# Performance work log

Hardware: AMD Instinct MI355X
Metric: run time of the kernel (lower is better)

Reference implementation:

```python
import jax, jax.numpy as jnp
import numpy as np

N = 10000        # nodes
F_IN = 128       # node features (data.num_node_features)
OUT = 16         # out_channels
H = 32           # attention heads
C1 = 4 * OUT     # hidden per-head dim (4*out_channels)
E = 80000        # directed edges
EPS = 1e-5       # BatchNorm eps
NEG = 0.2        # GATConv LeakyReLU negative_slope


def _gat(x, src, dst, W, a_s, a_d, b, n, C):
    # PyG GATConv, shared lin, concat=False (mean over heads)
    h = (x @ W).reshape(n, H, C)                    # [n,H,C]
    e_src = jnp.sum(h * a_s, -1)                    # [n,H] (alpha from x_j)
    e_dst = jnp.sum(h * a_d, -1)                    # [n,H] (alpha from x_i)
    e = jax.nn.leaky_relu(e_src[src] + e_dst[dst], NEG)     # [E',H]
    m = jax.ops.segment_max(e, dst, num_segments=n)         # segment softmax
    p = jnp.exp(e - m[dst])
    z = jax.ops.segment_sum(p, dst, num_segments=n)
    alpha = p / z[dst]
    out = jax.ops.segment_sum(alpha[:, :, None] * h[src], dst, num_segments=n)
    return out.mean(1) + b                          # mean over heads + bias


def _bn(x, g, b, m, v):  # eval-mode BatchNorm1d (running stats)
    return (x - m) * g / jnp.sqrt(v + EPS) + b


def setup_inputs():
    k = jax.random.split(jax.random.key(0), 40)
    rn = lambda i, s, sc=0.1: jax.random.normal(k[i], s, jnp.float32) * sc
    d = {"x": jax.random.normal(k[0], (N, F_IN), jnp.float32),
         "edge_index": jax.random.randint(k[1], (2, E), 0, N, jnp.int32)}
    # 4 GATConv layers
    d.update(W1=rn(2, (F_IN, H * C1)), as1=rn(3, (H, C1)), ad1=rn(4, (H, C1)), b1=rn(5, (C1,)))
    d.update(W2=rn(6, (C1, H * OUT)), as2=rn(7, (H, OUT)), ad2=rn(8, (H, OUT)), b2=rn(9, (OUT,)))
    d.update(W3=rn(10, (F_IN, H * C1)), as3=rn(11, (H, C1)), ad3=rn(12, (H, C1)), b3=rn(13, (C1,)))
    d.update(W4=rn(14, (C1, H * OUT)), as4=rn(15, (H, OUT)), ad4=rn(16, (H, OUT)), b4=rn(17, (OUT,)))
    # ResidualNetwork(1 block): 1x1 Conv1d over L=1 == matmul
    d.update(rwa=rn(18, (F_IN, OUT)), rba=rn(19, (OUT,)),
             bn1g=jnp.ones(OUT), bn1b=jnp.zeros(OUT), bn1m=rn(20, (OUT,)), bn1v=jnp.abs(rn(21, (OUT,))) + 1.0,
             rwb=rn(22, (OUT, OUT)), rbb=rn(23, (OUT,)),
             bn2g=jnp.ones(OUT), bn2b=jnp.zeros(OUT), bn2m=rn(24, (OUT,)), bn2v=jnp.abs(rn(25, (OUT,))) + 1.0,
             wsc=rn(26, (F_IN, OUT)), bsc=rn(27, (OUT,)),
             bnsg=jnp.ones(OUT), bnsb=jnp.zeros(OUT), bnsm=rn(28, (OUT,)), bnsv=jnp.abs(rn(29, (OUT,))) + 1.0,
             wfc=rn(30, (OUT, OUT)), bfc=rn(31, (OUT,)))
    return d


def reference(x, edge_index, W1, as1, ad1, b1, W2, as2, ad2, b2,
              W3, as3, ad3, b3, W4, as4, ad4, b4,
              rwa, rba, bn1g, bn1b, bn1m, bn1v, rwb, rbb, bn2g, bn2b, bn2m, bn2v,
              wsc, bsc, bnsg, bnsb, bnsm, bnsv, wfc, bfc):
    n = x.shape[0]
    loops = jnp.arange(n, dtype=edge_index.dtype)  # add_self_loops=True
    s2t_src = jnp.concatenate([edge_index[0], loops])  # flow source_to_target
    s2t_dst = jnp.concatenate([edge_index[1], loops])
    t2s_src = jnp.concatenate([edge_index[1], loops])  # flow target_to_source
    t2s_dst = jnp.concatenate([edge_index[0], loops])
    # dropout in original is unassigned (no-op); eval mode assumed
    x_s = jax.nn.elu(_gat(x, s2t_src, s2t_dst, W1, as1, ad1, b1, n, C1))
    x_in = jax.nn.elu(_gat(x_s, s2t_src, s2t_dst, W2, as2, ad2, b2, n, OUT))
    x_t = jax.nn.elu(_gat(x, t2s_src, t2s_dst, W3, as3, ad3, b3, n, C1))
    x_out = jax.nn.elu(_gat(x_t, t2s_src, t2s_dst, W4, as4, ad4, b4, n, OUT))
    # ResidualNetwork: block + identity avg-pool (L=1) + fc
    h = jax.nn.relu(_bn(x @ rwa + rba, bn1g, bn1b, bn1m, bn1v))
    h = _bn(h @ rwb + rbb, bn2g, bn2b, bn2m, bn2v)
    sc = _bn(x @ wsc + bsc, bnsg, bnsb, bnsm, bnsv)
    x_self = jax.nn.relu(h + sc) @ wfc + bfc
    return (x_in, x_out, x_self)
```

## Files before the change

### kernel.cpp

```cpp
#include <hip/hip_runtime.h>
#include <stdint.h>

__device__ __forceinline__ float bf2f(unsigned short u) {
  union { unsigned int i; float f; } v; v.i = ((unsigned int)u) << 16; return v.f;
}
__device__ __forceinline__ unsigned short f2bf(float f) {
  union { float f; unsigned int i; } v; v.f = f;
  unsigned int i = v.i;
  unsigned int r = (i + 0x7fffu + ((i >> 16) & 1u)) >> 16;
  return (unsigned short)r;
}

typedef __bf16 bf16x8 __attribute__((ext_vector_type(8)));
typedef float f32x4 __attribute__((ext_vector_type(4)));
typedef float f32x2 __attribute__((ext_vector_type(2)));
union ABfrag { int4 i4; bf16x8 v; };

#if __has_builtin(__builtin_amdgcn_cvt_pk_fp8_f32) && __has_builtin(__builtin_amdgcn_cvt_pk_f32_fp8)
#define HW_FP8 1
#else
#define HW_FP8 0
#endif

__device__ __forceinline__ unsigned char f2fp8_sw(float f) {
  union { float f; unsigned int u; } v; v.f = f;
  unsigned int s = (v.u >> 24) & 0x80;
  float a = fabsf(f);
  if (a >= 448.f) return (unsigned char)(s | 0x7E);
  v.f = a;
  int ex = (int)(v.u >> 23);
  unsigned int man = v.u & 0x7FFFFFu;
  if (ex >= 121) {
    unsigned int val = ((unsigned int)(ex - 120) << 3) | (man >> 20);
    unsigned int rem = man & 0xFFFFFu;
    if (rem > 0x80000u || (rem == 0x80000u && (val & 1))) val++;
    if (val > 0x7E) val = 0x7E;
    return (unsigned char)(s | val);
  }
  int q = (int)(a * 512.f + 0.5f);
  if (q > 8) q = 8;
  return (unsigned char)(s | (unsigned int)q);
}
__device__ __forceinline__ float fp8dec_sw(unsigned char c) {
  unsigned int e = (c >> 3) & 15u, m = c & 7u;
  float v;
  if (e) { union { unsigned int u; float f; } x; x.u = ((e + 120) << 23) | (m << 20); v = x.f; }
  else v = (float)m * 0.001953125f;
  return (c & 0x80) ? -v : v;
}
__device__ __forceinline__ unsigned int pack4_fp8(float a0, float a1, float a2, float a3) {
#if HW_FP8
  int dw = __builtin_amdgcn_cvt_pk_fp8_f32(a0, a1, 0, false);
  dw = __builtin_amdgcn_cvt_pk_fp8_f32(a2, a3, dw, true);
  return (unsigned int)dw;
#else
  return (unsigned)f2fp8_sw(a0) | ((unsigned)f2fp8_sw(a1) << 8) |
         ((unsigned)f2fp8_sw(a2) << 16) | ((unsigned)f2fp8_sw(a3) << 24);
#endif
}
__device__ __forceinline__ unsigned int bytesel4(uint4 v, int rr) {
#if __has_builtin(__builtin_amdgcn_perm)
  unsigned s = (unsigned)rr | ((unsigned)(rr + 4) << 8);
  unsigned p01 = __builtin_amdgcn_perm(v.y, v.x, s);
  unsigned p23 = __builtin_amdgcn_perm(v.w, v.z, s);
  return __builtin_amdgcn_perm(p23, p01, 0x05040100u);
#else
  int sh = rr * 8;
  return ((v.x >> sh) & 0xFFu) | (((v.y >> sh) & 0xFFu) << 8) |
         (((v.z >> sh) & 0xFFu) << 16) | (((v.w >> sh) & 0xFFu) << 24);
#endif
}
__device__ __forceinline__ void dec16p(int4 g, f32x2 o[8]) {
#if HW_FP8
  o[0] = __builtin_amdgcn_cvt_pk_f32_fp8(g.x, false);
  o[1] = __builtin_amdgcn_cvt_pk_f32_fp8(g.x, true);
  o[2] = __builtin_amdgcn_cvt_pk_f32_fp8(g.y, false);
  o[3] = __builtin_amdgcn_cvt_pk_f32_fp8(g.y, true);
  o[4] = __builtin_amdgcn_cvt_pk_f32_fp8(g.z, false);
  o[5] = __builtin_amdgcn_cvt_pk_f32_fp8(g.z, true);
  o[6] = __builtin_amdgcn_cvt_pk_f32_fp8(g.w, false);
  o[7] = __builtin_amdgcn_cvt_pk_f32_fp8(g.w, true);
#else
  unsigned int w[4] = {(unsigned)g.x, (unsigned)g.y, (unsigned)g.z, (unsigned)g.w};
#pragma unroll
  for (int d = 0; d < 4; ++d) {
    unsigned int x = w[d];
    o[d * 2 + 0] = (f32x2){fp8dec_sw((unsigned char)(x & 0xFF)),
                           fp8dec_sw((unsigned char)((x >> 8) & 0xFF))};
    o[d * 2 + 1] = (f32x2){fp8dec_sw((unsigned char)((x >> 16) & 0xFF)),
                           fp8dec_sw((unsigned char)((x >> 24) & 0xFF))};
  }
#endif
}

__device__ __forceinline__ float lrelu_clamp(float e) {
  e = (e > 0.f) ? e : 0.2f * e;
  return fminf(e, 80.f);
}

__global__ __launch_bounds__(256) void k_detect(const unsigned int* __restrict__ x, int* flag,
                                                int* __restrict__ degAB, int ndeg2) {
  if (blockIdx.x == 0) {
    __shared__ int cnt;
    if (threadIdx.x == 0) cnt = 0;
    __syncthreads();
    int c = 0;
    for (int i = threadIdx.x; i < 1024; i += 256) {
      unsigned int lo = x[i] & 0xFFFFu;
      int ex = (int)((lo >> 7) & 0xFF);
      if (ex >= 100 && ex <= 140) c++;
    }
    atomicAdd(&cnt, c);
    __syncthreads();
    if (threadIdx.x == 0) flag[0] = (cnt > 600) ? 1 : 0;
    return;
  }
  for (int idx = (blockIdx.x - 1) * 256 + threadIdx.x; idx < ndeg2; idx += 8 * 256) degAB[idx] = 0;
}

struct PrepDesc {
  const void* csrc[32]; float* cdst[32]; int cn[32];
  const void* x; float* xc; unsigned short* xp;
  const void* W1; const void* W2; const void* W3; const void* W4;
  unsigned short* P1; unsigned short* P2; unsigned short* P3; unsigned short* P4;
  int* degAB;
  const int* ei;
  const void* av[4];
  float* wa[4];
  int nxb, xtotal, ctotal, E, nn;
};
__global__ __launch_bounds__(256) void k_prep(PrepDesc d, const int* __restrict__ flag) {
  int isbf = *flag;
  int b = blockIdx.x;
  if (b < d.nxb) {
    int t8 = b * 256 + threadIdx.x;
    int i8 = t8 * 8;
    if (i8 < d.xtotal) {
      float v[8];
      if (isbf) {
        int4 raw = *(const int4*)((const unsigned short*)d.x + i8);
        const unsigned short* u = (const unsigned short*)&raw;
#pragma unroll
        for (int j = 0; j < 8; ++j) v[j] = bf2f(u[j]);
      } else {
        float4 f0 = *(const float4*)((const float*)d.x + i8);
        float4 f1 = *(const float4*)((const float*)d.x + i8 + 4);
        v[0] = f0.x; v[1] = f0.y; v[2] = f0.z; v[3] = f0.w;
        v[4] = f1.x; v[5] = f1.y; v[6] = f1.z; v[7] = f1.w;
      }
      *(float4*)(d.xc + i8)     = (float4){v[0], v[1], v[2], v[3]};
      *(float4*)(d.xc + i8 + 4) = (float4){v[4], v[5], v[6], v[7]};
      int row = i8 >> 7, c0 = i8 & 127;
      int tm = row >> 4, mr = row & 15;
      int s = c0 >> 5, quad = (c0 >> 3) & 3;
      unsigned short o[8];
#pragma unroll
      for (int j = 0; j < 8; ++j) o[j] = f2bf(v[j]);
      size_t idx = (((size_t)tm * 4 + s) * 64 + quad * 16 + mr) * 8;
      *(int4*)(d.xp + idx) = *(const int4*)o;
    }
    return;
  }
  b -= d.nxb;
  if (b < 288) {
    int u = b * 256 + threadIdx.x;
    const void* W; unsigned short* P; int K, N, lu;
    if (u < 32768)      { W = d.W1; P = d.P1; K = 128; N = 2048; lu = u; }
    else if (u < 36864) { W = d.W2; P = d.P2; K = 64;  N = 512;  lu = u - 32768; }
    else if (u < 69632) { W = d.W3; P = d.P3; K = 128; N = 2048; lu = u - 36864; }
    else                { W = d.W4; P = d.P4; K = 64;  N = 512;  lu = u - 69632; }
    int ksteps = K >> 5;
    int g = lu / (ksteps * 64);
    int rem = lu - g * (ksteps * 64);
    int s = rem >> 6, lane = rem & 63;
    int mr = lane & 15, quad = lane >> 4;
    int col = g * 16 + mr;
    int kbase = s * 32 + quad * 8;
#pragma unroll
    for (int j = 0; j < 8; ++j) {
      size_t src = (size_t)(kbase + j) * N + col;
      float v = isbf ? bf2f(((const unsigned short*)W)[src]) : ((const float*)W)[src];
      P[(size_t)lu * 8 + j] = f2bf(v);
    }
    return;
  }
  b -= 288;
  if (b < 32) {
    int t = b;
    int nels = d.cn[t];
    const void* src = d.csrc[t];
    float* dst = d.cdst[t];
    for (int idx = threadIdx.x; idx < nels; idx += 256) {
      float v = isbf ? bf2f(((const unsigned short*)src)[idx])
                     : ((const float*)src)[idx];
      dst[idx] = v;
    }
    return;
  }
  b -= 32;
  {
    int degblks = (d.E + 255) >> 8;
    if (b < degblks) {
      int e = b * 256 + threadIdx.x;
      if (e < d.E) {
        atomicAdd(&d.degAB[d.ei[d.E + e]], 1);
        atomicAdd(&d.degAB[d.nn + d.ei[e]], 1);
      }
      return;
    }
    b -= degblks;
  }
  {
    int m = b >> 4, kb = b & 15;
    const void* W = (m < 2) ? d.W1 : d.W3;
    const void* A = d.av[m];
    float* out = d.wa[m];
    int k = kb * 8 + (threadIdx.x >> 5);
    int h = threadIdx.x & 31;
    size_t wbase = (size_t)k * 2048 + h * 64;
    size_t abase = (size_t)h * 64;
    float acc = 0.f;
    if (isbf) {
      const unsigned short* Wb = (const unsigned short*)W;
      const unsigned short* Ab = (const unsigned short*)A;
#pragma unroll
      for (int v8 = 0; v8 < 8; ++v8) {
        int4 wv = *(const int4*)(Wb + wbase + v8 * 8);
        int4 av = *(const int4*)(Ab + abase + v8 * 8);
        const unsigned short* wu = (const unsigned short*)&wv;
        const unsigned short* au = (const unsigned short*)&av;
#pragma unroll
        for (int j = 0; j < 8; ++j) acc += bf2f(wu[j]) * bf2f(au[j]);
      }
    } else {
      const float* Wf = (const float*)W;
      const float* Af = (const float*)A;
#pragma unroll
      for (int v4 = 0; v4 < 16; ++v4) {
        float4 wv = *(const float4*)(Wf + wbase + v4 * 4);
        float4 av = *(const float4*)(Af + abase + v4 * 4);
        acc += wv.x * av.x + wv.y * av.y + wv.z * av.z + wv.w * av.w;
      }
    }
    out[k * 32 + h] = acc;
  }
}

__global__ __launch_bounds__(1024) void k_exscan2(const int* __restrict__ degA, const int* __restrict__ degB,
                                                  int* __restrict__ rowA, int* __restrict__ rowB,
                                                  int* __restrict__ colA, int* __restrict__ colB,
                                                  int* __restrict__ curA, int* __restrict__ curB, int n) {
  const int* deg = (blockIdx.x == 0) ? degA : degB;
  int* row = (blockIdx.x == 0) ? rowA : rowB;
  int* colx = (blockIdx.x == 0) ? colA : colB;
  int* curx = (blockIdx.x == 0) ? curA : curB;
  __shared__ int wsum[16], wbase[16];
  __shared__ int carry;
  if (threadIdx.x == 0) carry = 0;
  __syncthreads();
  int lane = threadIdx.x & 63, w = threadIdx.x >> 6;
  int chunks = (n + 1023) >> 10;
  for (int ch = 0; ch < chunks; ++ch) {
    int i = (ch << 10) + threadIdx.x;
    int v = (i < n) ? deg[i] : 0;
    int sc = v;
#pragma unroll
    for (int o = 1; o < 64; o <<= 1) { int t = __shfl_up(sc, o); if (lane >= o) sc += t; }
    if (lane == 63) wsum[w] = sc;
    __syncthreads();
    if (threadIdx.x < 16) {
      int v2 = wsum[threadIdx.x], s2 = v2;
#pragma unroll
      for (int o = 1; o < 16; o <<= 1) { int t = __shfl_up(s2, o); if (lane >= o) s2 += t; }
      wbase[threadIdx.x] = s2 - v2;
      if (threadIdx.x == 15) wsum[15] = s2;
    }
    __syncthreads();
    if (i < n) {
      int rv = carry + wbase[w] + (sc - v) + i;
      row[i] = rv;
      colx[rv] = i;
      curx[i] = rv + 1;
    }
    __syncthreads();
    if (threadIdx.x == 0) carry += wsum[15];
    __syncthreads();
  }
  if (threadIdx.x == 0) row[n] = carry + n;
}

#define TILE_DW 288
template<int CH, int KSTEPS>
__device__ __forceinline__ void mm_es64_body(int rg, int cg, int MT,
    const unsigned short* __restrict__ Ap, const unsigned short* __restrict__ Bp,
    unsigned char* __restrict__ C, const float* __restrict__ a_s, const float* __restrict__ a_d,
    float* __restrict__ es, float* __restrict__ ed, int N, unsigned int* tile) {
  const int TI = KSTEPS * 64;
  int vt = MT - rg * 4; if (vt > 4) vt = 4;
  int wid = threadIdx.x >> 6;
  int tn = cg * 4 + wid;
  int lane = threadIdx.x & 63;
  int mr = lane & 15, quad = lane >> 4;
  const int4* ap = (const int4*)(Ap + (size_t)rg * 4 * TI * 8) + lane;
  const unsigned short* bp = Bp + ((size_t)tn * 4 * KSTEPS) * 512 + lane * 8;
  unsigned int* twave = tile + wid * TILE_DW;
  f32x4 acc[4][4];
#pragma unroll
  for (int rt = 0; rt < 4; ++rt)
#pragma unroll
    for (int nt = 0; nt < 4; ++nt) acc[rt][nt] = (f32x4){0.f, 0.f, 0.f, 0.f};
#pragma unroll
  for (int s = 0; s < KSTEPS; ++s) {
    ABfrag bfr[4];
#pragma unroll
    for (int nt = 0; nt < 4; ++nt) bfr[nt].i4 = *(const int4*)(bp + (size_t)(nt * KSTEPS + s) * 512);
    ABfrag afr[4];
#pragma unroll
    for (int rt = 0; rt < 4; ++rt) {
      int rti = (rt < vt) ? rt : 0;
      afr[rt].i4 = ap[rti * TI + s * 64];
    }
#pragma unroll
    for (int nt = 0; nt < 4; ++nt)
#pragma unroll
      for (int rt = 0; rt < 4; ++rt)
        acc[rt][nt] = __builtin_amdgcn_mfma_f32_16x16x32_bf16(afr[rt].v, bfr[nt].v, acc[rt][nt], 0, 0, 0);
  }
  int r16 = lane >> 2, seg = lane & 3;
  int qr = r16 >> 2, rr = r16 & 3;
#pragma unroll
  for (int rt = 0; rt < 4; ++rt) {
    if (rt < vt) {
      int tm = rg * 4 + rt;
#pragma unroll
      for (int nt = 0; nt < 4; ++nt) {
        unsigned int dwv = pack4_fp8(acc[rt][nt][0], acc[rt][nt][1], acc[rt][nt][2], acc[rt][nt][3]);
        twave[quad * 72 + nt * 16 + mr] = dwv;
      }
      unsigned int out[4];
#pragma unroll
      for (int w = 0; w < 4; ++w) {
        uint4 v = *(const uint4*)&twave[qr * 72 + seg * 16 + 4 * w];
        out[w] = bytesel4(v, rr);
      }
      *(int4*)(C + (size_t)(tm * 16 + r16) * N + tn * 64 + seg * 16) = *(const int4*)out;
    }
  }
  if (CH == 16) {
    float ws[4], wd[4];
#pragma unroll
    for (int nt = 0; nt < 4; ++nt) {
      ws[nt] = a_s[(tn * 4 + nt) * 16 + mr];
      wd[nt] = a_d[(tn * 4 + nt) * 16 + mr];
    }
#pragma unroll
    for (int rt = 0; rt < 4; ++rt) {
      if (rt < vt) {
        int tm = rg * 4 + rt;
        float pes[4][4], ped[4][4];
#pragma unroll
        for (int nt = 0; nt < 4; ++nt)
#pragma unroll
          for (int r = 0; r < 4; ++r) { pes[nt][r] = acc[rt][nt][r] * ws[nt]; ped[nt][r] = acc[rt][nt][r] * wd[nt]; }
#pragma unroll
        for (int m = 1; m < 16; m <<= 1)
#pragma unroll
          for (int nt = 0; nt < 4; ++nt)
#pragma unroll
            for (int r = 0; r < 4; ++r) {
              pes[nt][r] += __shfl_xor(pes[nt][r], m);
              ped[nt][r] += __shfl_xor(ped[nt][r], m);
            }
        if (mr == 0) {
#pragma unroll
          for (int nt = 0; nt < 4; ++nt)
#pragma unroll
            for (int r = 0; r < 4; ++r) {
              int row = tm * 16 + quad * 4 + r;
              es[row * 32 + tn * 4 + nt] = pes[nt][r];
              ed[row * 32 + tn * 4 + nt] = ped[nt][r];
            }
        }
      }
    }
  }
}

union SM13 {
  struct { float xs[16][128]; float ha[16][16]; float tt[16][16]; } res;
  unsigned int tile[4 * TILE_DW];
};
struct MM13XDesc {
  int resblks, sblks, mmblks, mt, E;
  const int* ei; int* colA; int* colB; int* curA; int* curB;
  const float* xc;
  const float* rp[20];
  const float* wa[4];
  float* es1; float* ed1; float* es3; float* ed3;
  void* outbase; size_t eoff; int n;
  const int* flag;
  const unsigned short* Ap;
  const unsigned short* B1; const unsigned short* B3;
  unsigned char* C1; unsigned char* C3;
};
__global__ __launch_bounds__(256) void k_mm13x(MM13XDesc d) {
  __shared__ SM13 sm;
  int b = blockIdx.x;
  if (b < d.resblks) {
    int nodebase = b * 16;
    for (int t = threadIdx.x; t < 16 * 128; t += 256)
      sm.res.xs[t >> 7][t & 127] = d.xc[(size_t)(nodebase + (t >> 7)) * 128 + (t & 127)];
    __syncthreads();
    int ni = threadIdx.x >> 4, c = threadIdx.x & 15;
    {
      const float* w0 = d.wa[0]; const float* w1 = d.wa[1];
      const float* w2 = d.wa[2]; const float* w3 = d.wa[3];
      float a0 = 0.f, a1 = 0.f, a2 = 0.f, a3 = 0.f, a4 = 0.f, a5 = 0.f, a6 = 0.f, a7 = 0.f;
#pragma unroll 4
      for (int k = 0; k < 128; ++k) {
        float xv = sm.res.xs[ni][k];
        int o = k * 32 + c;
        a0 += xv * w0[o]; a1 += xv * w0[o + 16];
        a2 += xv * w1[o]; a3 += xv * w1[o + 16];
        a4 += xv * w2[o]; a5 += xv * w2[o + 16];
        a6 += xv * w3[o]; a7 += xv * w3[o + 16];
      }
      int row = nodebase + ni;
      d.es1[row * 32 + c] = a0; d.es1[row * 32 + c + 16] = a1;
      d.ed1[row * 32 + c] = a2; d.ed1[row * 32 + c + 16] = a3;
      d.es3[row * 32 + c] = a4; d.es3[row * 32 + c + 16] = a5;
      d.ed3[row * 32 + c] = a6; d.ed3[row * 32 + c + 16] = a7;
    }
    const float* rwa = d.rp[0]; const float* rba = d.rp[1];
    const float* bn1g = d.rp[2]; const float* bn1b = d.rp[3];
    const float* bn1m = d.rp[4]; const float* bn1v = d.rp[5];
    const float* rwb = d.rp[6]; const float* rbb = d.rp[7];
    const float* bn2g = d.rp[8]; const float* bn2b = d.rp[9];
    const float* bn2m = d.rp[10]; const float* bn2v = d.rp[11];
    const float* wsc = d.rp[12]; const float* bsc = d.rp[13];
    const float* bnsg = d.rp[14]; const float* bnsb = d.rp[15];
    const float* bnsm = d.rp[16]; const float* bnsv = d.rp[17];
    const float* wfc = d.rp[18]; const float* bfc = d.rp[19];
    float ya = 0.f, ysc = 0.f;
#pragma unroll 8
    for (int k = 0; k < 128; ++k) {
      float xv = sm.res.xs[ni][k];
      ya  += xv * rwa[k * 16 + c];
      ysc += xv * wsc[k * 16 + c];
    }
    ya += rba[c]; ysc += bsc[c];
    float s1 = bn1g[c] * rsqrtf(bn1v[c] + 1e-5f);
    ya = (ya - bn1m[c]) * s1 + bn1b[c];
    ya = fmaxf(ya, 0.f);
    float ss = bnsg[c] * rsqrtf(bnsv[c] + 1e-5f);
    ysc = (ysc - bnsm[c]) * ss + bnsb[c];
    sm.res.ha[ni][c] = ya;
    __syncthreads();
    float h2 = rbb[c];
#pragma unroll
    for (int k = 0; k < 16; ++k) h2 += sm.res.ha[ni][k] * rwb[k * 16 + c];
    float s2 = bn2g[c] * rsqrtf(bn2v[c] + 1e-5f);
    h2 = (h2 - bn2m[c]) * s2 + bn2b[c];
    sm.res.tt[ni][c] = fmaxf(h2 + ysc, 0.f);
    __syncthreads();
    float o = bfc[c];
#pragma unroll
    for (int k = 0; k < 16; ++k) o += sm.res.tt[ni][k] * wfc[k * 16 + c];
    size_t oo = d.eoff + (size_t)(nodebase + ni) * 16 + c;
    if (*d.flag) ((unsigned short*)d.outbase)[oo] = f2bf(o);
    else         ((float*)d.outbase)[oo] = o;
    return;
  }
  b -= d.resblks;
  if (b < d.sblks) {
    int e = b * 256 + threadIdx.x;
    if (e < d.E) {
      int s = d.ei[e], dd = d.ei[d.E + e];
      d.colA[atomicAdd(&d.curA[dd], 1)] = s;
      d.colB[atomicAdd(&d.curB[s], 1)] = dd;
    }
    return;
  }
  b -= d.sblks;
  if (b < d.mmblks) {
    mm_es64_body<64,4>(b >> 3, b & 7, d.mt, d.Ap, d.B1, d.C1, nullptr, nullptr, nullptr, nullptr, 2048, sm.tile);
    return;
  }
  b -= d.mmblks;
  mm_es64_body<64,4>(b >> 3, b & 7, d.mt, d.Ap, d.B3, d.C3, nullptr, nullptr, nullptr, nullptr, 2048, sm.tile);
}

__global__ __launch_bounds__(256) void k_g64(const unsigned char* __restrict__ h1,
                                             const unsigned char* __restrict__ h3,
                                             const float* __restrict__ es1, const float* __restrict__ ed1,
                                             const float* __restrict__ es3, const float* __restrict__ ed3,
                                             const int* __restrict__ rowA, const int* __restrict__ colA,
                                             const int* __restrict__ rowB, const int* __restrict__ colB,
                                             const float* __restrict__ b1, const float* __restrict__ b3,
                                             unsigned short* __restrict__ xsp, unsigned short* __restrict__ xtp,
                                             int n, int gb) {
  __shared__ float part[2][2][64];
  int b = blockIdx.x;
  const unsigned char* h; const float *es, *ed, *bias; const int *rowp, *col; unsigned short* outp;
  if (b < gb) { h = h1; es = es1; ed = ed1; rowp = rowA; col = colA; bias = b1; outp = xsp; }
  else { b -= gb; h = h3; es = es3; ed = ed3; rowp = rowB; col = colB; bias = b3; outp = xtp; }
  int wid = threadIdx.x >> 6, lane = threadIdx.x & 63;
  int nb = wid >> 1, half = wid & 1;
  int i = b * 2 + nb;
  bool active = (i < n);
  int hd = half * 16 + (lane >> 2);
  float e0 = 0.f;
  int beg = 0, deg = 0;
  if (active) {
    e0 = ed[i * 32 + hd];
    beg = rowp[i];
    deg = rowp[i + 1] - beg;
  }
  int colv = (lane < deg) ? col[beg + lane] : 0;
  f32x2 acc[8];
#pragma unroll
  for (int k = 0; k < 8; ++k) acc[k] = (f32x2){0.f, 0.f};
  float Z = 0.f;
  if (active) {
    int s0 = __shfl(colv, 0);
    const int4* hp = (const int4*)(h + (size_t)s0 * 2048 + (size_t)half * 1024);
    int4 ng = hp[lane];
    float ne = es[s0 * 32 + hd];
    for (int j = 0; j < deg; ++j) {
      int4 g = ng; float ee = ne;
      int jn = j + 1;
      if (jn < deg) {
        int sn = (jn < 64) ? __shfl(colv, jn) : col[beg + jn];
        const int4* hq = (const int4*)(h + (size_t)sn * 2048 + (size_t)half * 1024);
        ng = hq[lane];
        ne = es[sn * 32 + hd];
      }
      float q = __expf(lrelu_clamp(ee + e0));
      Z += q;
      f32x2 d[8];
      dec16p(g, d);
      f32x2 qv = (f32x2){q, q};
#pragma unroll
      for (int k = 0; k < 8; ++k) acc[k] = __builtin_elementwise_fma(qv, d[k], acc[k]);
    }
  }
  float zi = active ? (1.0f / Z) : 0.f;
  f32x2 ziv = (f32x2){zi, zi};
  f32x2 v2[8];
#pragma unroll
  for (int k = 0; k < 8; ++k) v2[k] = acc[k] * ziv;
#pragma unroll
  for (int m = 4; m < 64; m <<= 1)
#pragma unroll
    for (int k = 0; k < 8; ++k) {
      v2[k].x += __shfl_xor(v2[k].x, m);
      v2[k].y += __shfl_xor(v2[k].y, m);
    }
  if (lane < 4) {
#pragma unroll
    for (int k = 0; k < 8; ++k)
      *(float2*)&part[nb][half][lane * 16 + 2 * k] = (float2){v2[k].x, v2[k].y};
  }
  __syncthreads();
  if (half == 0 && lane < 4 && active) {
    float v[16];
#pragma unroll
    for (int k = 0; k < 16; ++k)
      v[k] = part[nb][0][lane * 16 + k] + part[nb][1][lane * 16 + k];
    int tm = i >> 4, mr = i & 15;
    unsigned short ob[16];
#pragma unroll
    for (int k = 0; k < 16; ++k) {
      float t = v[k] * (1.f / 32.f) + bias[lane * 16 + k];
      t = (t > 0.f) ? t : (__expf(t) - 1.f);
      ob[k] = f2bf(t);
    }
    int s0w = lane >> 1;
#pragma unroll
    for (int g2 = 0; g2 < 2; ++g2) {
      size_t idx = (((size_t)tm * 2 + s0w) * 64 + ((lane & 1) * 2 + g2) * 16 + mr) * 8;
      *(int4*)(outp + idx) = *(const int4*)(ob + g2 * 8);
    }
  }
}

__global__ __launch_bounds__(256) void k_mm24(const unsigned short* __restrict__ xsp,
                                              const unsigned short* __restrict__ xtp,
                                              const unsigned short* __restrict__ W2p,
                                              const unsigned short* __restrict__ W4p,
                                              unsigned char* __restrict__ h2, unsigned char* __restrict__ h4,
                                              const float* __restrict__ as2, const float* __restrict__ ad2,
                                              const float* __restrict__ as4, const float* __restrict__ ad4,
                                              float* __restrict__ es2, float* __restrict__ ed2,
                                              float* __restrict__ es4, float* __restrict__ ed4,
                                              int mmblks, int mt) {
  __shared__ unsigned int tile[4 * TILE_DW];
  int b = blockIdx.x;
  if (b < mmblks)
    mm_es64_body<16,2>(b >> 1, b & 1, mt, xsp, W2p, h2, as2, ad2, es2, ed2, 512, tile);
  else {
    b -= mmblks;
    mm_es64_body<16,2>(b >> 1, b & 1, mt, xtp, W4p, h4, as4, ad4, es4, ed4, 512, tile);
  }
}

__global__ __launch_bounds__(256) void k_g16(const unsigned char* __restrict__ h2,
                                             const unsigned char* __restrict__ h4,
                                             const float* __restrict__ es2, const float* __restrict__ ed2,
                                             const float* __restrict__ es4, const float* __restrict__ ed4,
                                             const int* __restrict__ rowA, const int* __restrict__ colA,
                                             const int* __restrict__ rowB, const int* __restrict__ colB,
                                             const float* __restrict__ b2, const float* __restrict__ b4,
                                             void* __restrict__ outbase, int n, int gb,
                                             const int* __restrict__ flag) {
  int b = blockIdx.x;
  const unsigned char* h; const float *es, *ed, *bias; const int *rowp, *col; size_t eoff;
  if (b < gb) { h = h2; es = es2; ed = ed2; rowp = rowA; col = colA; bias = b2; eoff = 0; }
  else { b -= gb; h = h4; es = es4; ed = ed4; rowp = rowB; col = colB; bias = b4; eoff = (size_t)n * 16; }
  int wid = threadIdx.x >> 6, lane = threadIdx.x & 63;
  int i = b * 4 + wid;
  if (i >= n) return;
  int hh = lane & 31, j2 = lane >> 5;
  float ev = ed[i * 32 + hh];
  int beg = rowp[i], end = rowp[i + 1];
  int deg = end - beg;
  int colv = (lane < deg) ? col[beg + lane] : 0;
  f32x2 acc[8];
#pragma unroll
  for (int k = 0; k < 8; ++k) acc[k] = (f32x2){0.f, 0.f};
  float Z = 0.f;
  int j = j2;
  int4 ng = (int4){0, 0, 0, 0};
  float ne = 0.f;
  if (j < deg) {
    int s = __shfl(colv, j);
    ng = ((const int4*)(h + (size_t)s * 512))[hh];
    ne = es[s * 32 + hh];
  }
  for (; j < deg; j += 2) {
    int4 g = ng; float ee = ne;
    int jn = j + 2;
    if (jn < deg) {
      int sn = (jn < 64) ? __shfl(colv, jn) : col[beg + jn];
      ng = ((const int4*)(h + (size_t)sn * 512))[hh];
      ne = es[sn * 32 + hh];
    }
    float q = __expf(lrelu_clamp(ee + ev));
    Z += q;
    f32x2 d[8];
    dec16p(g, d);
    f32x2 qv = (f32x2){q, q};
#pragma unroll
    for (int k = 0; k < 8; ++k) acc[k] = __builtin_elementwise_fma(qv, d[k], acc[k]);
  }
  Z += __shfl_xor(Z, 32);
  float zi = 1.0f / Z;
  f32x2 ziv = (f32x2){zi, zi};
  f32x2 v2[8];
#pragma unroll
  for (int k = 0; k < 8; ++k) v2[k] = acc[k] * ziv;
#pragma unroll
  for (int m = 1; m < 64; m <<= 1)
#pragma unroll
    for (int k = 0; k < 8; ++k) {
      v2[k].x += __shfl_xor(v2[k].x, m);
      v2[k].y += __shfl_xor(v2[k].y, m);
    }
  if (lane == 0) {
    float v[16];
#pragma unroll
    for (int k = 0; k < 8; ++k) { v[2 * k] = v2[k].x; v[2 * k + 1] = v2[k].y; }
    int isbf = *flag;
    if (isbf) {
      unsigned short ob[16];
#pragma unroll
      for (int k = 0; k < 16; ++k) {
        float t = v[k] * (1.f / 32.f) + bias[k];
        t = (t > 0.f) ? t : (__expf(t) - 1.f);
        ob[k] = f2bf(t);
      }
      unsigned short* o = (unsigned short*)outbase + eoff + (size_t)i * 16;
      *(int4*)o = *(const int4*)ob;
      *(int4*)(o + 8) = *(const int4*)(ob + 8);
    } else {
      float* o = (float*)outbase + eoff + (size_t)i * 16;
#pragma unroll
      for (int k = 0; k < 16; ++k) {
        float t = v[k] * (1.f / 32.f) + bias[k];
        t = (t > 0.f) ? t : (__expf(t) - 1.f);
        o[k] = t;
      }
    }
  }
}

extern "C" void kernel_launch(void* const* d_in, const int* in_sizes, int n_in,
                              void* d_out, int out_size, void* d_ws, size_t ws_size,
                              hipStream_t stream) {
  const int n = in_sizes[0] / 128;
  const int E = in_sizes[1] / 2;
  const int* ei = (const int*)d_in[1];

  char* wsp = (char*)d_ws; size_t off = 0;
  auto alloc = [&](size_t bytes) -> void* {
    void* p = wsp + off; off = (off + bytes + 255) & ~(size_t)255; return p;
  };
  int* flag = (int*)alloc(4);
  float* xc = (float*)alloc((size_t)n * 128 * 4);
  unsigned short* xp = (unsigned short*)alloc((size_t)n * 128 * 2);
  unsigned short* W1p = (unsigned short*)alloc((size_t)2048 * 128 * 2);
  unsigned short* W2p = (unsigned short*)alloc((size_t)512 * 64 * 2);
  unsigned short* W3p = (unsigned short*)alloc((size_t)2048 * 128 * 2);
  unsigned short* W4p = (unsigned short*)alloc((size_t)512 * 64 * 2);
  unsigned char* h1 = (unsigned char*)alloc((size_t)n * 2048);
  unsigned char* h3 = (unsigned char*)alloc((size_t)n * 2048);
  unsigned char* h2 = (unsigned char*)alloc((size_t)n * 512);
  unsigned char* h4 = (unsigned char*)alloc((size_t)n * 512);
  float* es1 = (float*)alloc((size_t)n * 32 * 4);
  float* ed1 = (float*)alloc((size_t)n * 32 * 4);
  float* es3 = (float*)alloc((size_t)n * 32 * 4);
  float* ed3 = (float*)alloc((size_t)n * 32 * 4);
  float* es2 = (float*)alloc((size_t)n * 32 * 4);
  float* ed2 = (float*)alloc((size_t)n * 32 * 4);
  float* es4 = (float*)alloc((size_t)n * 32 * 4);
  float* ed4 = (float*)alloc((size_t)n * 32 * 4);
  unsigned short* xsp = (unsigned short*)alloc((size_t)n * 64 * 2);
  unsigned short* xtp = (unsigned short*)alloc((size_t)n * 64 * 2);
  int* rowA = (int*)alloc((size_t)(n + 1) * 4);
  int* rowB = (int*)alloc((size_t)(n + 1) * 4);
  int* colA = (int*)alloc((size_t)(E + n) * 4);
  int* colB = (int*)alloc((size_t)(E + n) * 4);
  int* degAB = (int*)alloc((size_t)2 * n * 4);
  int* degA = degAB, * degB = degAB + n;
  int* curA = (int*)alloc((size_t)n * 4);
  int* curB = (int*)alloc((size_t)n * 4);
  float* was1 = (float*)alloc((size_t)128 * 32 * 4);
  float* wad1 = (float*)alloc((size_t)128 * 32 * 4);
  float* was3 = (float*)alloc((size_t)128 * 32 * 4);
  float* wad3 = (float*)alloc((size_t)128 * 32 * 4);

  static const int cidx[32] = {3,4,5, 7,8,9, 11,12,13, 15,16,17,
                               18,19,20,21,22,23,24,25,26,27,28,29,
                               30,31,32,33,34,35,36,37};
  PrepDesc pd;
  float* canon[38] = {nullptr};
  pd.ctotal = 0;
  for (int t = 0; t < 32; ++t) {
    int ii = cidx[t];
    canon[ii] = (float*)alloc((size_t)in_sizes[ii] * 4);
    pd.csrc[t] = d_in[ii];
    pd.cdst[t] = canon[ii];
    pd.cn[t] = in_sizes[ii];
    pd.ctotal += in_sizes[ii];
  }
  pd.x = d_in[0]; pd.xc = xc; pd.xp = xp;
  pd.W1 = d_in[2]; pd.W2 = d_in[6]; pd.W3 = d_in[10]; pd.W4 = d_in[14];
  pd.P1 = W1p; pd.P2 = W2p; pd.P3 = W3p; pd.P4 = W4p;
  pd.degAB = degAB;
  pd.ei = ei;
  pd.av[0] = d_in[3]; pd.av[1] = d_in[4]; pd.av[2] = d_in[11]; pd.av[3] = d_in[12];
  pd.wa[0] = was1; pd.wa[1] = wad1; pd.wa[2] = was3; pd.wa[3] = wad3;
  pd.nxb = (n * 128 / 8 + 255) / 256;
  pd.xtotal = n * 128;
  pd.E = E;
  pd.nn = n;
  (void)ws_size; (void)n_in; (void)out_size;

  const int degblks = (E + 255) / 256;

  k_detect<<<9, 256, 0, stream>>>((const unsigned int*)d_in[0], flag, degAB, 2 * n);
  k_prep<<<pd.nxb + 288 + 32 + degblks + 64, 256, 0, stream>>>(pd, flag);
  k_exscan2<<<2, 1024, 0, stream>>>(degA, degB, rowA, rowB, colA, colB, curA, curB, n);

  const int mt = n / 16;
  const int nrg = (mt + 3) / 4;
  const int mmblks64 = nrg * 8;
  const int mmblks16 = nrg * 2;
  const int gb2 = (n + 1) / 2;
  const int gb = (n + 3) / 4;

  MM13XDesc md;
  md.resblks = mt; md.sblks = degblks; md.mmblks = mmblks64; md.mt = mt; md.E = E;
  md.ei = ei; md.colA = colA; md.colB = colB; md.curA = curA; md.curB = curB;
  md.xc = xc;
  for (int t = 0; t < 20; ++t) md.rp[t] = canon[18 + t];
  md.wa[0] = was1; md.wa[1] = wad1; md.wa[2] = was3; md.wa[3] = wad3;
  md.es1 = es1; md.ed1 = ed1; md.es3 = es3; md.ed3 = ed3;
  md.outbase = d_out; md.eoff = (size_t)2 * n * 16; md.n = n; md.flag = flag;
  md.Ap = xp; md.B1 = W1p; md.B3 = W3p; md.C1 = h1; md.C3 = h3;
  k_mm13x<<<mt + degblks + 2 * mmblks64, 256, 0, stream>>>(md);

  k_g64<<<2 * gb2, 256, 0, stream>>>(h1, h3, es1, ed1, es3, ed3,
                                     rowA, colA, rowB, colB,
                                     canon[5], canon[13], xsp, xtp, n, gb2);
  k_mm24<<<2 * mmblks16, 256, 0, stream>>>(xsp, xtp, W2p, W4p, h2, h4,
                                           canon[7], canon[8], canon[15], canon[16],
                                           es2, ed2, es4, ed4, mmblks16, mt);
  k_g16<<<2 * gb, 256, 0, stream>>>(h2, h4, es2, ed2, es4, ed4,
                                    rowA, colA, rowB, colB,
                                    canon[9], canon[17], d_out, n, gb, flag);
}
```

Baseline: 314.2 us.

## Process one node per wave in k_g64, dropping shared-memory head-half reduction

The layer-1/3 aggregation kernel previously split each node's 32 heads across two waves, which combined partial sums through shared memory with a block barrier. Each wave now handles all 32 heads of one node, with two accumulator sets and two feature loads per edge, and blocks cover four nodes instead of two. This removes the LDS round trip, the __syncthreads and the duplicated edge-list and index work. In exchange it doubles per-thread registers and loads per iteration and halves the number of waves, which may reduce latency hiding.

Measured after the change: 306.5 us. 1.03x faster.

```diff
diff --git a/kernel.cpp b/kernel.cpp
--- a/kernel.cpp
+++ b/kernel.cpp
@@ -499,56 +499,59 @@
                                              const float* __restrict__ b1, const float* __restrict__ b3,
                                              unsigned short* __restrict__ xsp, unsigned short* __restrict__ xtp,
                                              int n, int gb) {
-  __shared__ float part[2][2][64];
   int b = blockIdx.x;
   const unsigned char* h; const float *es, *ed, *bias; const int *rowp, *col; unsigned short* outp;
   if (b < gb) { h = h1; es = es1; ed = ed1; rowp = rowA; col = colA; bias = b1; outp = xsp; }
   else { b -= gb; h = h3; es = es3; ed = ed3; rowp = rowB; col = colB; bias = b3; outp = xtp; }
   int wid = threadIdx.x >> 6, lane = threadIdx.x & 63;
-  int nb = wid >> 1, half = wid & 1;
-  int i = b * 2 + nb;
-  bool active = (i < n);
-  int hd = half * 16 + (lane >> 2);
-  float e0 = 0.f;
-  int beg = 0, deg = 0;
-  if (active) {
-    e0 = ed[i * 32 + hd];
-    beg = rowp[i];
-    deg = rowp[i + 1] - beg;
-  }
+  int i = b * 4 + wid;
+  if (i >= n) return;
+  int hd0 = lane >> 2, hd1 = 16 + hd0;
+  float e0 = ed[i * 32 + hd0];
+  float e1 = ed[i * 32 + hd1];
+  int beg = rowp[i], end = rowp[i + 1];
+  int deg = end - beg;
   int colv = (lane < deg) ? col[beg + lane] : 0;
-  f32x2 acc[8];
-#pragma unroll
-  for (int k = 0; k < 8; ++k) acc[k] = (f32x2){0.f, 0.f};
-  float Z = 0.f;
-  if (active) {
-    int s0 = __shfl(colv, 0);
-    const int4* hp = (const int4*)(h + (size_t)s0 * 2048 + (size_t)half * 1024);
-    int4 ng = hp[lane];
-    float ne = es[s0 * 32 + hd];
-    for (int j = 0; j < deg; ++j) {
-      int4 g = ng; float ee = ne;
-      int jn = j + 1;
-      if (jn < deg) {
-        int sn = (jn < 64) ? __shfl(colv, jn) : col[beg + jn];
-        const int4* hq = (const int4*)(h + (size_t)sn * 2048 + (size_t)half * 1024);
-        ng = hq[lane];
-        ne = es[sn * 32 + hd];
-      }
-      float q = __expf(lrelu_clamp(ee + e0));
-      Z += q;
-      f32x2 d[8];
-      dec16p(g, d);
-      f32x2 qv = (f32x2){q, q};
-#pragma unroll
-      for (int k = 0; k < 8; ++k) acc[k] = __builtin_elementwise_fma(qv, d[k], acc[k]);
-    }
-  }
-  float zi = active ? (1.0f / Z) : 0.f;
-  f32x2 ziv = (f32x2){zi, zi};
+  f32x2 acc0[8], acc1[8];
+#pragma unroll
+  for (int k = 0; k < 8; ++k) { acc0[k] = (f32x2){0.f, 0.f}; acc1[k] = (f32x2){0.f, 0.f}; }
+  float Z0 = 0.f, Z1 = 0.f;
+  int s0 = __shfl(colv, 0);
+  const int4* hp0 = (const int4*)(h + (size_t)s0 * 2048);
+  int4 ng0 = hp0[lane];
+  int4 ng1 = hp0[64 + lane];
+  float na = es[s0 * 32 + hd0];
+  float nb = es[s0 * 32 + hd1];
+  for (int j = 0; j < deg; ++j) {
+    int4 g0 = ng0, g1 = ng1;
+    float ea = na, eb = nb;
+    int jn = j + 1;
+    if (jn < deg) {
+      int sn = (jn < 64) ? __shfl(colv, jn) : col[beg + jn];
+      const int4* hq = (const int4*)(h + (size_t)sn * 2048);
+      ng0 = hq[lane];
+      ng1 = hq[64 + lane];
+      na = es[sn * 32 + hd0];
+      nb = es[sn * 32 + hd1];
+    }
+    float q0 = __expf(lrelu_clamp(ea + e0));
+    float q1 = __expf(lrelu_clamp(eb + e1));
+    Z0 += q0; Z1 += q1;
+    f32x2 d0[8], d1[8];
+    dec16p(g0, d0); dec16p(g1, d1);
+    f32x2 q0v = (f32x2){q0, q0}, q1v = (f32x2){q1, q1};
+#pragma unroll
+    for (int k = 0; k < 8; ++k) {
+      acc0[k] = __builtin_elementwise_fma(q0v, d0[k], acc0[k]);
+      acc1[k] = __builtin_elementwise_fma(q1v, d1[k], acc1[k]);
+    }
+  }
+  float zi0 = 1.0f / Z0, zi1 = 1.0f / Z1;
+  f32x2 zi0v = (f32x2){zi0, zi0}, zi1v = (f32x2){zi1, zi1};
   f32x2 v2[8];
 #pragma unroll
-  for (int k = 0; k < 8; ++k) v2[k] = acc[k] * ziv;
+  for (int k = 0; k < 8; ++k)
+    v2[k] = __builtin_elementwise_fma(acc1[k], zi1v, acc0[k] * zi0v);
 #pragma unroll
   for (int m = 4; m < 64; m <<= 1)
 #pragma unroll
@@ -557,16 +560,9 @@
       v2[k].y += __shfl_xor(v2[k].y, m);
     }
   if (lane < 4) {
-#pragma unroll
-    for (int k = 0; k < 8; ++k)
-      *(float2*)&part[nb][half][lane * 16 + 2 * k] = (float2){v2[k].x, v2[k].y};
-  }
-  __syncthreads();
-  if (half == 0 && lane < 4 && active) {
     float v[16];
 #pragma unroll
-    for (int k = 0; k < 16; ++k)
-      v[k] = part[nb][0][lane * 16 + k] + part[nb][1][lane * 16 + k];
+    for (int k = 0; k < 8; ++k) { v[2 * k] = v2[k].x; v[2 * k + 1] = v2[k].y; }
     int tm = i >> 4, mr = i & 15;
     unsigned short ob[16];
 #pragma unroll
@@ -776,7 +772,6 @@
   const int nrg = (mt + 3) / 4;
   const int mmblks64 = nrg * 8;
   const int mmblks16 = nrg * 2;
-  const int gb2 = (n + 1) / 2;
   const int gb = (n + 3) / 4;
 
   MM13XDesc md;
@@ -790,9 +785,9 @@
   md.Ap = xp; md.B1 = W1p; md.B3 = W3p; md.C1 = h1; md.C3 = h3;
   k_mm13x<<<mt + degblks + 2 * mmblks64, 256, 0, stream>>>(md);
 
-  k_g64<<<2 * gb2, 256, 0, stream>>>(h1, h3, es1, ed1, es3, ed3,
-                                     rowA, colA, rowB, colB,
-                                     canon[5], canon[13], xsp, xtp, n, gb2);
+  k_g64<<<2 * gb, 256, 0, stream>>>(h1, h3, es1, ed1, es3, ed3,
+                                    rowA, colA, rowB, colB,
+                                    canon[5], canon[13], xsp, xtp, n, gb);
   k_mm24<<<2 * mmblks16, 256, 0, stream>>>(xsp, xtp, W2p, W4p, h2, h4,
                                            canon[7], canon[8], canon[15], canon[16],
                                            es2, ed2, es4, ed4, mmblks16, mt);
```
